# Kernel tuning notes

Hardware: AMD Instinct MI355X
Metric: run time of the kernel (lower is better)

Reference implementation:

```python
import jax, jax.numpy as jnp
import numpy as np

BN_EPS = 1e-5

def _bn_relu(x, gamma, beta):
    # training-mode BatchNorm1d: biased batch stats over (B, N) per channel
    mean = x.mean(axis=(0, 2), keepdims=True)
    var = x.var(axis=(0, 2), keepdims=True)
    xn = (x - mean) * jax.lax.rsqrt(var + BN_EPS)
    return jax.nn.relu(xn * gamma[None, :, None] + beta[None, :, None])


def setup_inputs() -> dict:
    key = jax.random.key(0)
    ks = jax.random.split(key, 12)
    B, n1, n2, c1, c2 = 16, 4096, 1024, 128, 256
    in_ch, mlp = c1 + c2, [256, 128]
    xyz1 = jax.random.uniform(ks[0], (B, n1, 3), dtype=jnp.float32)
    xyz2 = jax.random.uniform(ks[1], (B, n2, 3), dtype=jnp.float32)
    feat1 = jax.random.normal(ks[2], (B, c1, n1), dtype=jnp.float32)
    feat2 = jax.random.normal(ks[3], (B, c2, n2), dtype=jnp.float32)
    # Conv1d(k=1) weights as (out, in) matrices; kaiming-ish scale
    w0 = jax.random.normal(ks[4], (mlp[0], in_ch), dtype=jnp.float32) / np.sqrt(in_ch)
    b0 = jnp.zeros((mlp[0],), jnp.float32)
    g0 = jnp.ones((mlp[0],), jnp.float32)
    be0 = jnp.zeros((mlp[0],), jnp.float32)
    w1 = jax.random.normal(ks[5], (mlp[1], mlp[0]), dtype=jnp.float32) / np.sqrt(mlp[0])
    b1 = jnp.zeros((mlp[1],), jnp.float32)
    g1 = jnp.ones((mlp[1],), jnp.float32)
    be1 = jnp.zeros((mlp[1],), jnp.float32)
    return {"xyz1": xyz1, "xyz2": xyz2, "feat1": feat1, "feat2": feat2,
            "w0": w0, "b0": b0, "g0": g0, "be0": be0,
            "w1": w1, "b1": b1, "g1": g1, "be1": be1}


def reference(xyz1, xyz2, feat1, feat2, w0, b0, g0, be0, w1, b1, g1, be1):
    # three_nn_interpolate: squared pairwise dists (B, n1, n2)
    d = jnp.sum((xyz1[:, :, None, :] - xyz2[:, None, :, :]) ** 2, axis=-1)
    neg_d3, idx3 = jax.lax.top_k(-d, 3)          # 3 smallest dists
    d3 = -neg_d3                                  # (B, n1, 3)
    w = 1.0 / (d3 + 1e-8)
    w = w / jnp.sum(w, axis=-1, keepdims=True)
    # gather feat2 at knn indices: (B, c2, n1, 3)
    gathered = jnp.take_along_axis(feat2[:, :, None, :], idx3[:, None, :, :], axis=3)
    interp = jnp.sum(gathered * w[:, None, :, :], axis=-1)  # (B, c2, n1)

    x = jnp.concatenate([feat1, interp], axis=1)            # (B, c1+c2, n1)
    x = _bn_relu(jnp.einsum('oc,bcn->bon', w0, x) + b0[None, :, None], g0, be0)
    x = _bn_relu(jnp.einsum('oc,bcn->bon', w1, x) + b1[None, :, None], g1, be1)
    return x
```

## Files before the change

### kernel.cpp

```cpp
#include <hip/hip_runtime.h>
#include <hip/hip_bf16.h>

typedef unsigned short u16;
typedef __attribute__((ext_vector_type(8))) __bf16 bf16x8;
typedef __attribute__((ext_vector_type(4))) float floatx4;

#define B_   16
#define N1_  4096
#define N2_  1024
#define C1_  128
#define C2_  256
#define CIN_ 384
#define CM_  256
#define CO_  128

__device__ __forceinline__ u16 f2bf(float f) {
  unsigned u = __float_as_uint(f);
  u = (u + 0x7fffu + ((u >> 16) & 1u)) >> 16;
  return (u16)u;
}
__device__ __forceinline__ float bf2f(u16 h) {
  return __uint_as_float(((unsigned)h) << 16);
}

union U128 { uint4 u; bf16x8 v; u16 s[8]; };

__device__ __forceinline__ bf16x8 ldfrag(const u16* p) {
  U128 x; x.u = *(const uint4*)p; return x.v;
}
__device__ __forceinline__ uint4 pack8(const u16* h) {
  uint4 u;
  u.x = (unsigned)h[0] | ((unsigned)h[1] << 16);
  u.y = (unsigned)h[2] | ((unsigned)h[3] << 16);
  u.z = (unsigned)h[4] | ((unsigned)h[5] << 16);
  u.w = (unsigned)h[6] | ((unsigned)h[7] << 16);
  return u;
}


__global__ __launch_bounds__(256) void castw_kernel(
    const float* __restrict__ w0, const float* __restrict__ w1,
    u16* __restrict__ w0b, u16* __restrict__ w1b)
{
  int i = blockIdx.x * 256 + threadIdx.x;
  if (i < 12288) {
    int m = i / 48, kc = i % 48;
    const float* p = w0 + m * CIN_ + kc * 8;
    u16 h8[8];
    #pragma unroll
    for (int j = 0; j < 8; ++j) h8[j] = f2bf(p[j]);
    int mt = m >> 4, col = m & 15, kt = kc >> 2, quad = kc & 3;
    *(uint4*)(w0b + ((mt*12 + kt)*512 + (quad*16 + col)*8)) = pack8(h8);
  } else {
    int i2 = i - 12288;
    int m = i2 >> 5, kc = i2 & 31;
    const float* p = w1 + m * CM_ + kc * 8;
    u16 h8[8];
    #pragma unroll
    for (int j = 0; j < 8; ++j) h8[j] = f2bf(p[j]);
    int mt = m >> 4, col = m & 15, kt = kc >> 2, quad = kc & 3;
    *(uint4*)(w1b + ((mt*8 + kt)*512 + (quad*16 + col)*8)) = pack8(h8);
  }
}

__global__ __launch_bounds__(256) void knn_part_kernel(
    const float* __restrict__ xyz1, const float* __restrict__ xyz2,
    float* __restrict__ pd, int* __restrict__ pi)
{
  __shared__ float4 sp[256];
  int b = blockIdx.y;
  int chunk = blockIdx.z;
  int t = threadIdx.x;
  const float* p2 = xyz2 + ((size_t)b * N2_ + chunk * 256) * 3;
  sp[t] = make_float4(p2[t*3], p2[t*3+1], p2[t*3+2], 0.f);
  __syncthreads();
  int i = blockIdx.x * 256 + t;
  const float* p1 = xyz1 + ((size_t)b * N1_ + i) * 3;
  float x = p1[0], y = p1[1], z = p1[2];
  float d0 = 1e30f, d1 = 1e30f, d2 = 1e30f;
  int i0 = 0, i1 = 0, i2 = 0;
  int jbase = chunk * 256;
  #pragma unroll 4
  for (int j = 0; j < 256; ++j) {
    float4 p = sp[j];
    float dx = x - p.x, dy = y - p.y, dz = z - p.z;
    float d = dx*dx + dy*dy + dz*dz;
    if (d < d2) {
      if (d < d0)      { d2=d1; i2=i1; d1=d0; i1=i0; d0=d; i0=jbase+j; }
      else if (d < d1) { d2=d1; i2=i1; d1=d;  i1=jbase+j; }
      else             { d2=d;  i2=jbase+j; }
    }
  }
  int o = chunk*65536 + b*4096 + i;
  pd[o] = d0; pd[o + 262144] = d1; pd[o + 524288] = d2;
  pi[o] = i0; pi[o + 262144] = i1; pi[o + 524288] = i2;
}

__global__ __launch_bounds__(256) void knn_merge_kernel(
    const float* __restrict__ pd, const int* __restrict__ pi,
    int* __restrict__ idx_out, float* __restrict__ w_out)
{
  int p = blockIdx.x * 256 + threadIdx.x;
  float d0 = 1e30f, d1 = 1e30f, d2 = 1e30f;
  int i0 = 0, i1 = 0, i2 = 0;
  #pragma unroll
  for (int c = 0; c < 4; ++c) {
    int o = c*65536 + p;
    #pragma unroll
    for (int k = 0; k < 3; ++k) {
      float d = pd[o + k*262144];
      int ix = pi[o + k*262144];
      if (d < d2) {
        if (d < d0)      { d2=d1; i2=i1; d1=d0; i1=i0; d0=d; i0=ix; }
        else if (d < d1) { d2=d1; i2=i1; d1=d;  i1=ix; }
        else             { d2=d;  i2=ix; }
      }
    }
  }
  float w0 = 1.f/(d0+1e-8f), w1 = 1.f/(d1+1e-8f), w2 = 1.f/(d2+1e-8f);
  float inv = 1.f/(w0+w1+w2);
  idx_out[p]          = i0;
  idx_out[p +  65536] = i1;
  idx_out[p + 131072] = i2;
  w_out[p]            = w0*inv;
  w_out[p +  65536]   = w1*inv;
  w_out[p + 131072]   = w2*inv;
}

__global__ __launch_bounds__(256) void tr2_kernel(
    const float* __restrict__ feat2, float* __restrict__ feat2T)
{
  __shared__ float sA[64][257];
  int b = blockIdx.y;
  int n0 = blockIdx.x * 64;
  int t = threadIdx.x;
  #pragma unroll
  for (int j = 0; j < 16; ++j) {
    int flat4 = t + j * 256;
    int c = flat4 >> 4, nn4 = (flat4 & 15) * 4;
    float4 v = *(const float4*)(feat2 + ((size_t)b*C2_ + c)*N2_ + n0 + nn4);
    sA[nn4+0][c] = v.x; sA[nn4+1][c] = v.y; sA[nn4+2][c] = v.z; sA[nn4+3][c] = v.w;
  }
  __syncthreads();
  int nn = t & 63, chunk = t >> 6;
  float* dst = feat2T + ((size_t)b*N2_ + n0 + nn)*C2_ + chunk*64;
  #pragma unroll
  for (int g = 0; g < 16; ++g) {
    int c = chunk*64 + g*4;
    float4 v = make_float4(sA[nn][c], sA[nn][c+1], sA[nn][c+2], sA[nn][c+3]);
    *(float4*)(dst + g*4) = v;
  }
}

__global__ __launch_bounds__(256) void prep_kernel(
    const float* __restrict__ feat1, const float* __restrict__ feat2T,
    const int* __restrict__ idx_in, const float* __restrict__ w_in,
    u16* __restrict__ xcatT)
{
  __shared__ float sA[64][133];
  int b = blockIdx.y;
  int n0 = blockIdx.x * 64;
  int t = threadIdx.x;
  #pragma unroll
  for (int j = 0; j < 8; ++j) {
    int flat4 = t + j * 256;
    int c = flat4 >> 4, nn4 = (flat4 & 15) * 4;
    float4 v = *(const float4*)(feat1 + ((size_t)b*C1_ + c)*N1_ + n0 + nn4);
    sA[nn4+0][c] = v.x; sA[nn4+1][c] = v.y; sA[nn4+2][c] = v.z; sA[nn4+3][c] = v.w;
  }
  __syncthreads();
  int nn = t & 63, chunk = t >> 6;
  int n = n0 + nn, nt = n >> 4, col = n & 15;
  u16* tb = xcatT + ((size_t)b*256 + nt)*12*512;
  #pragma unroll
  for (int g = 0; g < 4; ++g) {
    int c0 = chunk*32 + g*8;
    u16 h8[8];
    #pragma unroll
    for (int j = 0; j < 8; ++j) h8[j] = f2bf(sA[nn][c0 + j]);
    *(uint4*)(tb + (size_t)chunk*512 + (g*16 + col)*8) = pack8(h8);
  }
  int base = b*N1_ + n;
  int i0 = idx_in[base], i1 = idx_in[base + B_*N1_], i2 = idx_in[base + 2*B_*N1_];
  float w0 = w_in[base], w1 = w_in[base + B_*N1_], w2 = w_in[base + 2*B_*N1_];
  const float* r0 = feat2T + ((size_t)b*N2_ + i0)*C2_ + chunk*64;
  const float* r1 = feat2T + ((size_t)b*N2_ + i1)*C2_ + chunk*64;
  const float* r2 = feat2T + ((size_t)b*N2_ + i2)*C2_ + chunk*64;
  #pragma unroll
  for (int h = 0; h < 8; ++h) {
    float4 a0 = *(const float4*)(r0 + h*8),     a1 = *(const float4*)(r0 + h*8 + 4);
    float4 b0 = *(const float4*)(r1 + h*8),     b1 = *(const float4*)(r1 + h*8 + 4);
    float4 c0 = *(const float4*)(r2 + h*8),     c1 = *(const float4*)(r2 + h*8 + 4);
    u16 h8[8];
    h8[0] = f2bf(w0*a0.x + w1*b0.x + w2*c0.x);
    h8[1] = f2bf(w0*a0.y + w1*b0.y + w2*c0.y);
    h8[2] = f2bf(w0*a0.z + w1*b0.z + w2*c0.z);
    h8[3] = f2bf(w0*a0.w + w1*b0.w + w2*c0.w);
    h8[4] = f2bf(w0*a1.x + w1*b1.x + w2*c1.x);
    h8[5] = f2bf(w0*a1.y + w1*b1.y + w2*c1.y);
    h8[6] = f2bf(w0*a1.z + w1*b1.z + w2*c1.z);
    h8[7] = f2bf(w0*a1.w + w1*b1.w + w2*c1.w);
    int c = C1_ + chunk*64 + h*8;
    int kt = c >> 5, quad = (c >> 3) & 3;
    *(uint4*)(tb + (size_t)kt*512 + (quad*16 + col)*8) = pack8(h8);
  }
}

__global__ __launch_bounds__(256) void gemm1_mfma(
    const u16* __restrict__ xcatT, const u16* __restrict__ w0b,
    const float* __restrict__ b0p, u16* __restrict__ y0T,
    float* __restrict__ p0)
{
  __shared__ float ps[4][64][2];
  int t = threadIdx.x;
  int wave = t >> 6, lane = t & 63;
  int col = lane & 15, quad = lane >> 4;
  int wm = wave >> 1, wn = wave & 1;
  int b = blockIdx.y;
  int mtb = blockIdx.z*8 + wm*4;
  int ntb = blockIdx.x*8 + wn*4;

  const u16* ap = w0b + lane*8;
  const u16* bp = xcatT + ((size_t)(b*256 + ntb)*12)*512 + lane*8;

  floatx4 acc[4][4] = {};
  bf16x8 af[4], bf[4], afn[4], bfn[4];
  #pragma unroll
  for (int i = 0; i < 4; ++i) {
    af[i] = ldfrag(ap + (size_t)((mtb+i)*12)*512);
    bf[i] = ldfrag(bp + (size_t)(i*12)*512);
  }
  #pragma unroll 1
  for (int kt = 1; kt < 12; ++kt) {
    #pragma unroll
    for (int i = 0; i < 4; ++i) afn[i] = ldfrag(ap + (size_t)((mtb+i)*12 + kt)*512);
    #pragma unroll
    for (int i = 0; i < 4; ++i) bfn[i] = ldfrag(bp + (size_t)(i*12 + kt)*512);
    #pragma unroll
    for (int mt = 0; mt < 4; ++mt)
      #pragma unroll
      for (int nt = 0; nt < 4; ++nt)
        acc[mt][nt] = __builtin_amdgcn_mfma_f32_16x16x32_bf16(af[mt], bf[nt], acc[mt][nt], 0, 0, 0);
    #pragma unroll
    for (int i = 0; i < 4; ++i) { af[i] = afn[i]; bf[i] = bfn[i]; }
  }
  #pragma unroll
  for (int mt = 0; mt < 4; ++mt)
    #pragma unroll
    for (int nt = 0; nt < 4; ++nt)
      acc[mt][nt] = __builtin_amdgcn_mfma_f32_16x16x32_bf16(af[mt], bf[nt], acc[mt][nt], 0, 0, 0);

  int m0 = blockIdx.z*128 + wm*64;
  #pragma unroll
  for (int mt = 0; mt < 4; ++mt) {
    float4 bias4 = *(const float4*)(b0p + m0 + mt*16 + quad*4);
    float bia[4] = {bias4.x, bias4.y, bias4.z, bias4.w};
    int kt_out = (m0 >> 5) + (mt >> 1);
    int quad_out = ((mt & 1) << 1) | (quad >> 1);
    int j0 = (quad & 1) * 4;
    float s[4] = {}, q[4] = {};
    #pragma unroll
    for (int nt = 0; nt < 4; ++nt) {
      int nt_g = ntb + nt;
      u16 h[4];
      #pragma unroll
      for (int r = 0; r < 4; ++r) {
        float v = acc[mt][nt][r] + bia[r];
        u16 hh = f2bf(v);
        float vr = bf2f(hh);
        h[r] = hh; s[r] += vr; q[r] += vr*vr;
      }
      *(ushort4*)(y0T + (((size_t)b*256 + nt_g)*8 + kt_out)*512 + (quad_out*16 + col)*8 + j0)
          = make_ushort4(h[0], h[1], h[2], h[3]);
    }
    #pragma unroll
    for (int r = 0; r < 4; ++r) {
      float ss = s[r], qq = q[r];
      #pragma unroll
      for (int msk = 1; msk < 16; msk <<= 1) { ss += __shfl_xor(ss, msk); qq += __shfl_xor(qq, msk); }
      if (col == 0) {
        ps[wave][mt*16 + quad*4 + r][0] = ss;
        ps[wave][mt*16 + quad*4 + r][1] = qq;
      }
    }
  }
  __syncthreads();
  {
    int c = t >> 1, k = t & 1;
    int wbase = (c >> 6) * 2, ch = c & 63;
    float v = ps[wbase][ch][k] + ps[wbase+1][ch][k];
    size_t l = (size_t)blockIdx.z*512 + blockIdx.y*32 + blockIdx.x;
    p0[l*256 + t] = v;
  }
}

__global__ __launch_bounds__(256) void stats_kernel(
    const float* __restrict__ p, const float* __restrict__ g,
    const float* __restrict__ be, float* __restrict__ scale,
    float* __restrict__ shift, int half_split)
{
  int c = blockIdx.x, t = threadIdx.x;
  size_t base = half_split ? ((size_t)(c >> 7) * 512 * 256 + (size_t)(c & 127) * 2)
                           : ((size_t)c * 2);
  float s = 0.f, q = 0.f;
  #pragma unroll
  for (int i = 0; i < 2; ++i) {
    float2 v = *(const float2*)(p + base + (size_t)(t + i*256) * 256);
    s += v.x; q += v.y;
  }
  #pragma unroll
  for (int m = 1; m < 64; m <<= 1) { s += __shfl_xor(s, m); q += __shfl_xor(q, m); }
  __shared__ float2 red[4];
  if ((t & 63) == 0) red[t >> 6] = make_float2(s, q);
  __syncthreads();
  if (t == 0) {
    float ss = red[0].x + red[1].x + red[2].x + red[3].x;
    float qq = red[0].y + red[1].y + red[2].y + red[3].y;
    float mu  = ss * (1.f/65536.f);
    float var = qq * (1.f/65536.f) - mu*mu;
    float a = g[c] * rsqrtf(var + 1e-5f);
    scale[c] = a; shift[c] = be[c] - mu*a;
  }
}

__global__ __launch_bounds__(256) void gemm2_mfma(
    const u16* __restrict__ y0T, const u16* __restrict__ w1b,
    const float* __restrict__ b1p,
    const float* __restrict__ scale0, const float* __restrict__ shift0,
    float* __restrict__ out, float* __restrict__ p1)
{
  __shared__ float a0s[CM_], bb0s[CM_];
  __shared__ float ps[4][64][2];
  int t = threadIdx.x;
  a0s[t] = scale0[t]; bb0s[t] = shift0[t];
  __syncthreads();
  int wave = t >> 6, lane = t & 63;
  int col = lane & 15, quad = lane >> 4;
  int wm = wave >> 1, wn = wave & 1;
  int b = blockIdx.y;
  int mtb = wm*4;
  int ntb = blockIdx.x*8 + wn*4;

  const u16* ap = w1b + lane*8;
  const u16* bp = y0T + ((size_t)(b*256 + ntb)*8)*512 + lane*8;

  floatx4 acc[4][4] = {};
  bf16x8 af[4], afn[4];
  U128 braw[4], brawn[4];
  #pragma unroll
  for (int i = 0; i < 4; ++i) {
    af[i] = ldfrag(ap + (size_t)((mtb+i)*8)*512);
    braw[i].u = *(const uint4*)(bp + (size_t)(i*8)*512);
  }
  #pragma unroll 1
  for (int kt = 1; kt < 8; ++kt) {
    #pragma unroll
    for (int i = 0; i < 4; ++i) afn[i] = ldfrag(ap + (size_t)((mtb+i)*8 + kt)*512);
    #pragma unroll
    for (int i = 0; i < 4; ++i) brawn[i].u = *(const uint4*)(bp + (size_t)(i*8 + kt)*512);
    int c0 = (kt-1)*32 + quad*8;
    float4 av0 = *(const float4*)&a0s[c0], av1 = *(const float4*)&a0s[c0+4];
    float4 bv0 = *(const float4*)&bb0s[c0], bv1 = *(const float4*)&bb0s[c0+4];
    float av[8] = {av0.x,av0.y,av0.z,av0.w,av1.x,av1.y,av1.z,av1.w};
    float bv[8] = {bv0.x,bv0.y,bv0.z,bv0.w,bv1.x,bv1.y,bv1.z,bv1.w};
    bf16x8 bfv[4];
    #pragma unroll
    for (int i = 0; i < 4; ++i) {
      u16 h8[8];
      #pragma unroll
      for (int j = 0; j < 8; ++j)
        h8[j] = f2bf(fmaxf(fmaf(bf2f(braw[i].s[j]), av[j], bv[j]), 0.f));
      U128 x; x.u = pack8(h8); bfv[i] = x.v;
    }
    #pragma unroll
    for (int mt = 0; mt < 4; ++mt)
      #pragma unroll
      for (int nt = 0; nt < 4; ++nt)
        acc[mt][nt] = __builtin_amdgcn_mfma_f32_16x16x32_bf16(af[mt], bfv[nt], acc[mt][nt], 0, 0, 0);
    #pragma unroll
    for (int i = 0; i < 4; ++i) { af[i] = afn[i]; braw[i] = brawn[i]; }
  }
  {
    int c0 = 7*32 + quad*8;
    float4 av0 = *(const float4*)&a0s[c0], av1 = *(const float4*)&a0s[c0+4];
    float4 bv0 = *(const float4*)&bb0s[c0], bv1 = *(const float4*)&bb0s[c0+4];
    float av[8] = {av0.x,av0.y,av0.z,av0.w,av1.x,av1.y,av1.z,av1.w};
    float bv[8] = {bv0.x,bv0.y,bv0.z,bv0.w,bv1.x,bv1.y,bv1.z,bv1.w};
    bf16x8 bfv[4];
    #pragma unroll
    for (int i = 0; i < 4; ++i) {
      u16 h8[8];
      #pragma unroll
      for (int j = 0; j < 8; ++j)
        h8[j] = f2bf(fmaxf(fmaf(bf2f(braw[i].s[j]), av[j], bv[j]), 0.f));
      U128 x; x.u = pack8(h8); bfv[i] = x.v;
    }
    #pragma unroll
    for (int mt = 0; mt < 4; ++mt)
      #pragma unroll
      for (int nt = 0; nt < 4; ++nt)
        acc[mt][nt] = __builtin_amdgcn_mfma_f32_16x16x32_bf16(af[mt], bfv[nt], acc[mt][nt], 0, 0, 0);
  }

  int m0 = wm*64;
  int n0 = blockIdx.x*128 + wn*64;
  #pragma unroll
  for (int mt = 0; mt < 4; ++mt) {
    float4 bias4 = *(const float4*)(b1p + m0 + mt*16 + quad*4);
    float bia[4] = {bias4.x, bias4.y, bias4.z, bias4.w};
    float s[4] = {}, q[4] = {};
    #pragma unroll
    for (int nt = 0; nt < 4; ++nt) {
      int n = n0 + nt*16 + col;
      #pragma unroll
      for (int r = 0; r < 4; ++r) {
        float v = acc[mt][nt][r] + bia[r];
        out[((size_t)b*CO_ + m0 + mt*16 + quad*4 + r)*N1_ + n] = v;
        s[r] += v; q[r] += v*v;
      }
    }
    #pragma unroll
    for (int r = 0; r < 4; ++r) {
      float ss = s[r], qq = q[r];
      #pragma unroll
      for (int msk = 1; msk < 16; msk <<= 1) { ss += __shfl_xor(ss, msk); qq += __shfl_xor(qq, msk); }
      if (col == 0) {
        ps[wave][mt*16 + quad*4 + r][0] = ss;
        ps[wave][mt*16 + quad*4 + r][1] = qq;
      }
    }
  }
  __syncthreads();
  {
    int c = t >> 1, k = t & 1;
    int wbase = (c >> 6) * 2, ch = c & 63;
    float v = ps[wbase][ch][k] + ps[wbase+1][ch][k];
    size_t l = (size_t)blockIdx.y*32 + blockIdx.x;
    p1[l*256 + t] = v;
  }
}

__global__ __launch_bounds__(256) void bnrelu_kernel(
    float* __restrict__ out, const float* __restrict__ scale1, const float* __restrict__ shift1)
{
  int idx = blockIdx.x * 256 + threadIdx.x;
  int c = (idx >> 10) & (CO_ - 1);
  float a = scale1[c];
  float bb = shift1[c];
  float4 v = ((const float4*)out)[idx];
  v.x = fmaxf(fmaf(v.x, a, bb), 0.f);
  v.y = fmaxf(fmaf(v.y, a, bb), 0.f);
  v.z = fmaxf(fmaf(v.z, a, bb), 0.f);
  v.w = fmaxf(fmaf(v.w, a, bb), 0.f);
  ((float4*)out)[idx] = v;
}

extern "C" void kernel_launch(void* const* d_in, const int* in_sizes, int n_in,
                              void* d_out, int out_size, void* d_ws, size_t ws_size,
                              hipStream_t stream)
{
  const float* xyz1  = (const float*)d_in[0];
  const float* xyz2  = (const float*)d_in[1];
  const float* feat1 = (const float*)d_in[2];
  const float* feat2 = (const float*)d_in[3];
  const float* w0    = (const float*)d_in[4];
  const float* b0    = (const float*)d_in[5];
  const float* g0    = (const float*)d_in[6];
  const float* be0   = (const float*)d_in[7];
  const float* w1    = (const float*)d_in[8];
  const float* b1    = (const float*)d_in[9];
  const float* g1    = (const float*)d_in[10];
  const float* be1   = (const float*)d_in[11];
  float* out = (float*)d_out;
  char* ws = (char*)d_ws;

  u16*   xcatT   = (u16*)ws;
  float* knn_pd  = (float*)ws;
  int*   knn_pi  = (int*)(ws + 3145728);
  u16*   y0T     = (u16*)(ws + 50331648);
  float* feat2T  = (float*)(ws + 50331648);
  u16*   w0b     = (u16*)(ws + 83886080);
  u16*   w1b     = (u16*)(ws + 84082688);
  int*   idx_buf = (int*)(ws + 84148224);
  float* w_buf   = (float*)(ws + 84934656);
  float* p0      = (float*)(ws + 85721088);
  float* p1      = (float*)(ws + 86769664);
  float* scale0  = (float*)(ws + 87293952);
  float* shift0  = scale0 + 256;
  float* scale1  = scale0 + 512;
  float* shift1  = scale0 + 640;

  castw_kernel   <<<64,              256, 0, stream>>>(w0, w1, w0b, w1b);
  knn_part_kernel<<<dim3(16,16,4),   256, 0, stream>>>(xyz1, xyz2, knn_pd, knn_pi);
  knn_merge_kernel<<<256,            256, 0, stream>>>(knn_pd, knn_pi, idx_buf, w_buf);
  tr2_kernel     <<<dim3(16,16),     256, 0, stream>>>(feat2, feat2T);
  prep_kernel    <<<dim3(64,16),     256, 0, stream>>>(feat1, feat2T, idx_buf, w_buf, xcatT);
  gemm1_mfma     <<<dim3(32,16,2),   256, 0, stream>>>(xcatT, w0b, b0, y0T, p0);
  stats_kernel   <<<256,             256, 0, stream>>>(p0, g0, be0, scale0, shift0, 1);
  gemm2_mfma     <<<dim3(32,16),     256, 0, stream>>>(y0T, w1b, b1, scale0, shift0, out, p1);
  stats_kernel   <<<128,             256, 0, stream>>>(p1, g1, be1, scale1, shift1, 0);
  bnrelu_kernel  <<<8192,            256, 0, stream>>>(out, scale1, shift1);
}
```

Measured before the change: 277.2 us.

## Store transposed feat2 as bf16 and split interpolation into its own gather kernel

The transposed feat2 buffer is now written in bf16 instead of fp32, which halves its write traffic and the gather traffic of the interpolation. The old prep kernel is split in two: one kernel transposes feat1 into xcatT, and a new interp2 kernel gathers the three neighbours with a 32-lane-per-point layout so each lane reads 16 contiguous bytes. This adds an extra kernel launch and a second rounding step (feat2 is rounded to bf16 before the weighted sum) in exchange for less memory traffic and more coalesced gathers.

Result: faster. 251.7 us (-9.2%).

```diff
diff --git a/kernel.cpp b/kernel.cpp
--- a/kernel.cpp
+++ b/kernel.cpp
@@ -128,7 +128,7 @@
 }
 
 __global__ __launch_bounds__(256) void tr2_kernel(
-    const float* __restrict__ feat2, float* __restrict__ feat2T)
+    const float* __restrict__ feat2, u16* __restrict__ feat2Tb)
 {
   __shared__ float sA[64][257];
   int b = blockIdx.y;
@@ -143,19 +143,18 @@
   }
   __syncthreads();
   int nn = t & 63, chunk = t >> 6;
-  float* dst = feat2T + ((size_t)b*N2_ + n0 + nn)*C2_ + chunk*64;
-  #pragma unroll
-  for (int g = 0; g < 16; ++g) {
-    int c = chunk*64 + g*4;
-    float4 v = make_float4(sA[nn][c], sA[nn][c+1], sA[nn][c+2], sA[nn][c+3]);
-    *(float4*)(dst + g*4) = v;
-  }
-}
-
-__global__ __launch_bounds__(256) void prep_kernel(
-    const float* __restrict__ feat1, const float* __restrict__ feat2T,
-    const int* __restrict__ idx_in, const float* __restrict__ w_in,
-    u16* __restrict__ xcatT)
+  u16* dst = feat2Tb + ((size_t)b*N2_ + n0 + nn)*C2_ + chunk*64;
+  #pragma unroll
+  for (int g = 0; g < 8; ++g) {
+    u16 h8[8];
+    #pragma unroll
+    for (int j = 0; j < 8; ++j) h8[j] = f2bf(sA[nn][chunk*64 + g*8 + j]);
+    *(uint4*)(dst + g*8) = pack8(h8);
+  }
+}
+
+__global__ __launch_bounds__(256) void prep1_kernel(
+    const float* __restrict__ feat1, u16* __restrict__ xcatT)
 {
   __shared__ float sA[64][133];
   int b = blockIdx.y;
@@ -180,29 +179,35 @@
     for (int j = 0; j < 8; ++j) h8[j] = f2bf(sA[nn][c0 + j]);
     *(uint4*)(tb + (size_t)chunk*512 + (g*16 + col)*8) = pack8(h8);
   }
-  int base = b*N1_ + n;
-  int i0 = idx_in[base], i1 = idx_in[base + B_*N1_], i2 = idx_in[base + 2*B_*N1_];
-  float w0 = w_in[base], w1 = w_in[base + B_*N1_], w2 = w_in[base + 2*B_*N1_];
-  const float* r0 = feat2T + ((size_t)b*N2_ + i0)*C2_ + chunk*64;
-  const float* r1 = feat2T + ((size_t)b*N2_ + i1)*C2_ + chunk*64;
-  const float* r2 = feat2T + ((size_t)b*N2_ + i2)*C2_ + chunk*64;
-  #pragma unroll
-  for (int h = 0; h < 8; ++h) {
-    float4 a0 = *(const float4*)(r0 + h*8),     a1 = *(const float4*)(r0 + h*8 + 4);
-    float4 b0 = *(const float4*)(r1 + h*8),     b1 = *(const float4*)(r1 + h*8 + 4);
-    float4 c0 = *(const float4*)(r2 + h*8),     c1 = *(const float4*)(r2 + h*8 + 4);
+}
+
+__global__ __launch_bounds__(256) void interp2_kernel(
+    const u16* __restrict__ feat2Tb, const int* __restrict__ idx_in,
+    const float* __restrict__ w_in, u16* __restrict__ xcatT)
+{
+  int b = blockIdx.y;
+  int p0 = blockIdx.x * 64;
+  int t = threadIdx.x;
+  int seg = t & 31;
+  int pl  = t >> 5;
+  #pragma unroll 2
+  for (int pass = 0; pass < 8; ++pass) {
+    int n = p0 + pass*8 + pl;
+    int base = b*N1_ + n;
+    int i0 = idx_in[base], i1 = idx_in[base + 65536], i2 = idx_in[base + 131072];
+    float w0 = w_in[base], w1 = w_in[base + 65536], w2 = w_in[base + 131072];
+    const u16* fb = feat2Tb + (size_t)b*N2_*C2_ + seg*8;
+    U128 a, c, d;
+    a.u = *(const uint4*)(fb + (size_t)i0*C2_);
+    c.u = *(const uint4*)(fb + (size_t)i1*C2_);
+    d.u = *(const uint4*)(fb + (size_t)i2*C2_);
     u16 h8[8];
-    h8[0] = f2bf(w0*a0.x + w1*b0.x + w2*c0.x);
-    h8[1] = f2bf(w0*a0.y + w1*b0.y + w2*c0.y);
-    h8[2] = f2bf(w0*a0.z + w1*b0.z + w2*c0.z);
-    h8[3] = f2bf(w0*a0.w + w1*b0.w + w2*c0.w);
-    h8[4] = f2bf(w0*a1.x + w1*b1.x + w2*c1.x);
-    h8[5] = f2bf(w0*a1.y + w1*b1.y + w2*c1.y);
-    h8[6] = f2bf(w0*a1.z + w1*b1.z + w2*c1.z);
-    h8[7] = f2bf(w0*a1.w + w1*b1.w + w2*c1.w);
-    int c = C1_ + chunk*64 + h*8;
-    int kt = c >> 5, quad = (c >> 3) & 3;
-    *(uint4*)(tb + (size_t)kt*512 + (quad*16 + col)*8) = pack8(h8);
+    #pragma unroll
+    for (int j = 0; j < 8; ++j)
+      h8[j] = f2bf(w0*bf2f(a.s[j]) + w1*bf2f(c.s[j]) + w2*bf2f(d.s[j]));
+    int nt = n >> 4, col = n & 15;
+    int kt = 4 + (seg >> 2), quad = seg & 3;
+    *(uint4*)(xcatT + (((size_t)b*256 + nt)*12 + kt)*512 + (quad*16 + col)*8) = pack8(h8);
   }
 }
 
@@ -478,7 +483,7 @@
   float* knn_pd  = (float*)ws;
   int*   knn_pi  = (int*)(ws + 3145728);
   u16*   y0T     = (u16*)(ws + 50331648);
-  float* feat2T  = (float*)(ws + 50331648);
+  u16*   feat2Tb = (u16*)(ws + 50331648);
   u16*   w0b     = (u16*)(ws + 83886080);
   u16*   w1b     = (u16*)(ws + 84082688);
   int*   idx_buf = (int*)(ws + 84148224);
@@ -490,14 +495,15 @@
   float* scale1  = scale0 + 512;
   float* shift1  = scale0 + 640;
 
-  castw_kernel   <<<64,              256, 0, stream>>>(w0, w1, w0b, w1b);
-  knn_part_kernel<<<dim3(16,16,4),   256, 0, stream>>>(xyz1, xyz2, knn_pd, knn_pi);
-  knn_merge_kernel<<<256,            256, 0, stream>>>(knn_pd, knn_pi, idx_buf, w_buf);
-  tr2_kernel     <<<dim3(16,16),     256, 0, stream>>>(feat2, feat2T);
-  prep_kernel    <<<dim3(64,16),     256, 0, stream>>>(feat1, feat2T, idx_buf, w_buf, xcatT);
-  gemm1_mfma     <<<dim3(32,16,2),   256, 0, stream>>>(xcatT, w0b, b0, y0T, p0);
-  stats_kernel   <<<256,             256, 0, stream>>>(p0, g0, be0, scale0, shift0, 1);
-  gemm2_mfma     <<<dim3(32,16),     256, 0, stream>>>(y0T, w1b, b1, scale0, shift0, out, p1);
-  stats_kernel   <<<128,             256, 0, stream>>>(p1, g1, be1, scale1, shift1, 0);
-  bnrelu_kernel  <<<8192,            256, 0, stream>>>(out, scale1, shift1);
-}
+  castw_kernel    <<<64,              256, 0, stream>>>(w0, w1, w0b, w1b);
+  knn_part_kernel <<<dim3(16,16,4),   256, 0, stream>>>(xyz1, xyz2, knn_pd, knn_pi);
+  knn_merge_kernel<<<256,             256, 0, stream>>>(knn_pd, knn_pi, idx_buf, w_buf);
+  tr2_kernel      <<<dim3(16,16),     256, 0, stream>>>(feat2, feat2Tb);
+  prep1_kernel    <<<dim3(64,16),     256, 0, stream>>>(feat1, xcatT);
+  interp2_kernel  <<<dim3(64,16),     256, 0, stream>>>(feat2Tb, idx_buf, w_buf, xcatT);
+  gemm1_mfma      <<<dim3(32,16,2),   256, 0, stream>>>(xcatT, w0b, b0, y0T, p0);
+  stats_kernel    <<<256,             256, 0, stream>>>(p0, g0, be0, scale0, shift0, 1);
+  gemm2_mfma      <<<dim3(32,16),     256, 0, stream>>>(y0T, w1b, b1, scale0, shift0, out, p1);
+  stats_kernel    <<<128,             256, 0, stream>>>(p1, g1, be1, scale1, shift1, 0);
+  bnrelu_kernel   <<<8192,            256, 0, stream>>>(out, scale1, shift1);
+}
```
